# Optimization experiments

Measured on AMD Instinct MI355X. Metric: run time of the kernel, lower is better.

Reference implementation:

```python
import jax, jax.numpy as jnp
import numpy as np

B, Cin, Cout = 2, 32, 16
D, H, W = 48, 64, 128
K = 3
EPS = 1e-5  # BatchNorm3d default eps


def setup_inputs() -> dict:
    key = jax.random.key(0)
    ks = jax.random.split(key, 6)
    return {
        "x": jax.random.normal(ks[0], (B, Cin, D, H, W), jnp.float32),
        "weight": jax.random.normal(ks[1], (Cout, Cin, K, K, K), jnp.float32) * 0.05,
        "gamma": jax.random.uniform(ks[2], (Cout,), jnp.float32, minval=0.5, maxval=1.5),
        "beta": jax.random.normal(ks[3], (Cout,), jnp.float32) * 0.1,
        "running_mean": jax.random.normal(ks[4], (Cout,), jnp.float32) * 0.1,
        "running_var": jax.random.uniform(ks[5], (Cout,), jnp.float32, minval=0.5, maxval=1.5),
    }


def _binarize(v):
    # forward: sign(v) in {-1, 0, +1}; backward (STE): hardtanh grad (pass-through on |v|<=1)
    clipped = jnp.clip(v, -1.0, 1.0)
    return clipped + jax.lax.stop_gradient(jnp.sign(v) - clipped)


def reference(x, weight, gamma, beta, running_mean, running_var):
    b, c, d, h, w = x.shape
    # trilinear upsample, scale (1,2,2), align_corners=False (half-pixel centers)
    x = jax.image.resize(x, (b, c, d, 2 * h, 2 * w), method="trilinear")
    # binarize activations and weights; XNOR-style per-output-channel scale alpha = mean|W|
    xb = _binarize(x)
    alpha = jnp.mean(jnp.abs(weight), axis=(1, 2, 3, 4), keepdims=True)  # [Cout,1,1,1,1]
    wb = _binarize(weight) * alpha
    y = jax.lax.conv_general_dilated(
        xb, wb,
        window_strides=(1, 1, 1),
        padding=[(1, 1), (1, 1), (1, 1)],
        dimension_numbers=("NCDHW", "OIDHW", "NCDHW"),
    )  # [B, Cout, D, 2H, 2W]
    # fused BatchNorm3d (inference form) + ReLU
    inv = gamma / jnp.sqrt(running_var + EPS)
    shift = beta - running_mean * inv
    y = y * inv[None, :, None, None, None] + shift[None, :, None, None, None]
    return jax.nn.relu(y)
```

## Files before the change

kernel.cpp:

```cpp
#include <hip/hip_runtime.h>
#include <hip/hip_bf16.h>
#include <stdint.h>

#define BB   2
#define CIN  32
#define COUT 16
#define DD   48
#define HIN  64
#define WIN  128
#define H2   128
#define W2   256
#define PLANE_WORDS (H2 * W2)

__global__ __launch_bounds__(512) void ibc3d_prep(
    const float* __restrict__ wgt, const float* __restrict__ gamma,
    const float* __restrict__ beta, const float* __restrict__ rmean,
    const float* __restrict__ rvar, uint32_t* __restrict__ bw,
    float* __restrict__ scale, float* __restrict__ shift)
{
    int t = threadIdx.x;
    if (t < 27 * 16) {
        int tap = t >> 4, co = t & 15;
        uint32_t word = 0;
        for (int ci = 0; ci < CIN; ++ci) {
            float v = wgt[(co * CIN + ci) * 27 + tap];
            word |= (v > 0.0f ? 1u : 0u) << ci;
        }
        bw[t] = word;
    }
    {
        int co   = t >> 5;
        int lane = t & 31;
        double p = 0.0;
        for (int k = 0; k < 27; ++k)
            p += fabs((double)wgt[co * (CIN * 27) + lane + 32 * k]);
#pragma unroll
        for (int s = 16; s >= 1; s >>= 1)
            p += __shfl_down(p, s, 32);
        if (lane == 0) {
            float alpha = (float)(p / (double)(CIN * 27));
            float inv = gamma[co] / sqrtf(rvar[co] + 1e-5f);
            scale[co] = alpha * inv;
            shift[co] = beta[co] - rmean[co] * inv;
        }
    }
}

__device__ __forceinline__ uint32_t pack_word(const float* __restrict__ x,
                                              int b, int d, int h2, int w2)
{
    int m = h2 >> 1, dh = h2 & 1;
    int n = w2 >> 1, dwp = w2 & 1;
    int rA = m + dh - 1;
    int rB = rA + 1;
    double wA = dh ? 0.75 : 0.25;
    double wB = 1.0 - wA;
    rA = rA < 0 ? 0 : rA;
    rB = rB > (HIN - 1) ? (HIN - 1) : rB;
    int cA = n + dwp - 1;
    int cB = cA + 1;
    double wC = dwp ? 0.75 : 0.25;
    double wD = 1.0 - wC;
    cA = cA < 0 ? 0 : cA;
    cB = cB > (WIN - 1) ? (WIN - 1) : cB;

    const float* xp = x + ((size_t)b * CIN * DD + d) * (HIN * WIN);
    int oA = rA * WIN, oB = rB * WIN;
    uint32_t word = 0;
    for (int ci = 0; ci < CIN; ++ci) {
        const float* xc = xp + (size_t)ci * (DD * HIN * WIN);
        float a0 = xc[oA + cA], a1 = xc[oA + cB];
        float b0 = xc[oB + cA], b1 = xc[oB + cB];
        double t0 = wA * (double)a0 + wB * (double)b0;
        double t1 = wA * (double)a1 + wB * (double)b1;
        double v  = wC * t0 + wD * t1;
        word |= (v >= 0.0 ? 1u : 0u) << ci;
    }
    return word;
}

__global__ __launch_bounds__(256) void ibc3d_packr8(
    const float* __restrict__ x, uint32_t* __restrict__ bx,
    int b_start, int nplanes)
{
    int per = gridDim.x >> 3;
    int bid = (blockIdx.x & 7) * per + (blockIdx.x >> 3);
    int idx = bid * 256 + threadIdx.x;
    int j  = idx & 31;
    int h2 = (idx >> 5) & (H2 - 1);
    int pl = idx >> 12;
    if (pl >= nplanes) return;
    int d  = pl % DD;
    int b  = b_start + pl / DD;

    int m = h2 >> 1, q = h2 & 1;
    int rT = q ? m : (m > 0 ? m - 1 : 0);
    int rB = q ? (m < HIN - 1 ? m + 1 : HIN - 1) : m;
    float wT = q ? 0.75f : 0.25f;
    float wB = 1.0f - wT;

    int c0 = 4 * j;
    int cl = c0 >= 2 ? c0 - 2 : 0;
    int cr = (c0 + 4 <= WIN - 2) ? c0 + 4 : WIN - 2;

    const float* xp = x + ((size_t)b * CIN * DD + d) * (HIN * WIN);
    int oT = rT * WIN, oB2 = rB * WIN;

    uint32_t w[8];
#pragma unroll
    for (int k = 0; k < 8; ++k) w[k] = 0u;

#pragma unroll 2
    for (int ci = 0; ci < CIN; ++ci) {
        const float* xc = xp + (size_t)ci * (DD * HIN * WIN);
        float cT[6], cB[6];
        {
            const float* rowT = xc + oT;
            float2 L = *(const float2*)(rowT + cl);
            float4 M = *(const float4*)(rowT + c0);
            float2 R = *(const float2*)(rowT + cr);
            cT[0] = (j > 0)  ? L.y : L.x;
            cT[1] = M.x; cT[2] = M.y; cT[3] = M.z; cT[4] = M.w;
            cT[5] = (j < 31) ? R.x : R.y;
        }
        {
            const float* rowB = xc + oB2;
            float2 L = *(const float2*)(rowB + cl);
            float4 M = *(const float4*)(rowB + c0);
            float2 R = *(const float2*)(rowB + cr);
            cB[0] = (j > 0)  ? L.y : L.x;
            cB[1] = M.x; cB[2] = M.y; cB[3] = M.z; cB[4] = M.w;
            cB[5] = (j < 31) ? R.x : R.y;
        }

        float v[8];
#pragma unroll
        for (int t = 0; t < 4; ++t) {
            float uT0 = 0.25f * cT[t]     + 0.75f * cT[t + 1];
            float uT1 = 0.75f * cT[t + 1] + 0.25f * cT[t + 2];
            float uB0 = 0.25f * cB[t]     + 0.75f * cB[t + 1];
            float uB1 = 0.75f * cB[t + 1] + 0.25f * cB[t + 2];
            v[2 * t]     = wT * uT0 + wB * uB0;
            v[2 * t + 1] = wT * uT1 + wB * uB1;
        }

        float amin = 3.4e38f;
#pragma unroll
        for (int k = 0; k < 8; ++k)
            amin = fminf(amin, fabsf(v[k]));

        if (__builtin_expect(amin < 1e-5f, 0)) {
            double dwT = (double)wT, dwB = 1.0 - (double)wT;
#pragma unroll
            for (int t = 0; t < 4; ++t) {
                double eT0 = 0.25 * (double)cT[t]     + 0.75 * (double)cT[t + 1];
                double eT1 = 0.75 * (double)cT[t + 1] + 0.25 * (double)cT[t + 2];
                double eB0 = 0.25 * (double)cB[t]     + 0.75 * (double)cB[t + 1];
                double eB1 = 0.75 * (double)cB[t + 1] + 0.25 * (double)cB[t + 2];
                uint32_t s0 = (dwT * eT0 + dwB * eB0) >= 0.0;
                uint32_t s1 = (dwT * eT1 + dwB * eB1) >= 0.0;
                w[2 * t]     |= s0 << ci;
                w[2 * t + 1] |= s1 << ci;
            }
        } else {
#pragma unroll
            for (int k = 0; k < 8; ++k)
                w[k] |= (v[k] >= 0.0f ? 1u : 0u) << ci;
        }
    }

    size_t base = (size_t)pl * PLANE_WORDS + (size_t)h2 * W2 + 8 * j;
    *(uint4*)(bx + base)     = make_uint4(w[0], w[1], w[2], w[3]);
    *(uint4*)(bx + base + 4) = make_uint4(w[4], w[5], w[6], w[7]);
}

__global__ __launch_bounds__(256) void ibc3d_conv6(
    const uint32_t* __restrict__ bx, const uint32_t* __restrict__ bwg,
    const float* __restrict__ scaleg, const float* __restrict__ shiftg,
    float* __restrict__ out, int b_start)
{
    int per = gridDim.x >> 3;
    int bid = (blockIdx.x & 7) * per + (blockIdx.x >> 3);

    int h2    = bid & (H2 - 1);
    int plane = bid >> 7;
    int d     = plane % DD;
    int b     = b_start + plane / DD;
    int w2    = threadIdx.x;

    int acc[16];
#pragma unroll
    for (int c = 0; c < 16; ++c) acc[c] = 0;

#pragma unroll
    for (int kd = 0; kd < 3; ++kd) {
        int dd = d + kd - 1;
        if (dd < 0 || dd >= DD) continue;
        const uint32_t* bxp = bx + (size_t)(plane + kd - 1) * PLANE_WORDS;
#pragma unroll
        for (int kh = 0; kh < 3; ++kh) {
            int hh = h2 + kh - 1;
            if (hh < 0 || hh >= H2) continue;
            const uint32_t* brow = bxp + hh * W2;
#pragma unroll
            for (int kw = 0; kw < 3; ++kw) {
                int ww = w2 + kw - 1;
                if (ww >= 0 && ww < W2) {
                    uint32_t word = brow[ww];
                    int tap = kd * 9 + kh * 3 + kw;
#pragma unroll
                    for (int co = 0; co < 16; ++co)
                        acc[co] += __popc(word ^ bwg[tap * 16 + co]);
                }
            }
        }
    }

    int nd = 1 + (d > 0)  + (d < DD - 1);
    int nh = 1 + (h2 > 0) + (h2 < H2 - 1);
    int nw = 1 + (w2 > 0) + (w2 < W2 - 1);
    float base = 32.0f * (float)(nd * nh * nw);

    size_t obase = (((size_t)(b * COUT) * DD + d) * H2 + h2) * W2 + w2;
#pragma unroll
    for (int co = 0; co < 16; ++co) {
        float y = (base - 2.0f * (float)acc[co]) * scaleg[co] + shiftg[co];
        y = y > 0.0f ? y : 0.0f;
        out[obase + (size_t)co * (DD * H2 * W2)] = y;
    }
}

__global__ __launch_bounds__(256) void ibc3d_fused(
    const float* __restrict__ x, const float* __restrict__ wgt,
    const float* __restrict__ gamma, const float* __restrict__ beta,
    const float* __restrict__ rmean, const float* __restrict__ rvar,
    float* __restrict__ out)
{
    __shared__ uint32_t sbw[27 * 16];
    __shared__ float sscale[16];
    __shared__ float sshift[16];
    __shared__ uint32_t sw[3][10][264];

    int tid = threadIdx.x;
    for (int t = tid; t < 27 * 16; t += 256) {
        int tap = t >> 4, co = t & 15;
        uint32_t word = 0;
        for (int ci = 0; ci < CIN; ++ci) {
            float v = wgt[(co * CIN + ci) * 27 + tap];
            word |= (v > 0.0f ? 1u : 0u) << ci;
        }
        sbw[t] = word;
    }
    if (tid < 16) {
        int co = tid;
        double s = 0.0;
        for (int i = 0; i < CIN * 27; ++i)
            s += fabs((double)wgt[co * CIN * 27 + i]);
        float alpha = (float)(s / (double)(CIN * 27));
        float inv = gamma[co] / sqrtf(rvar[co] + 1e-5f);
        sscale[co] = alpha * inv;
        sshift[co] = beta[co] - rmean[co] * inv;
    }

    int bid = blockIdx.x;
    int hq  = bid & 15;
    int r   = bid >> 4;
    int b   = r / DD;
    int d   = r % DD;
    int h2base = hq * 8;

    for (int i = tid; i < 3 * 10 * 258; i += 256) {
        int kd  = i / 2580;
        int rem = i - kd * 2580;
        int ri  = rem / 258;
        int ciw = rem - ri * 258;
        int dd = d + kd - 1;
        int h2 = h2base - 1 + ri;
        int w2 = ciw - 1;
        uint32_t word = 0;
        if (dd >= 0 && dd < DD && h2 >= 0 && h2 < H2 && w2 >= 0 && w2 < W2)
            word = pack_word(x, b, dd, h2, w2);
        sw[kd][ri][ciw] = word;
    }
    __syncthreads();

    int w2 = tid;
    for (int p = 0; p < 8; ++p) {
        int h2 = h2base + p;
        int acc[16];
#pragma unroll
        for (int c = 0; c < 16; ++c) acc[c] = 0;
        int nv = 0;
        for (int kd = 0; kd < 3; ++kd) {
            int dd = d + kd - 1;
            if (dd < 0 || dd >= DD) continue;
            for (int kh = 0; kh < 3; ++kh) {
                int hh = h2 + kh - 1;
                if (hh < 0 || hh >= H2) continue;
                for (int kw = 0; kw < 3; ++kw) {
                    int ww = w2 + kw - 1;
                    if (ww < 0 || ww >= W2) continue;
                    uint32_t word = sw[kd][p + kh][w2 + kw];
                    nv += 1;
                    int tap = kd * 9 + kh * 3 + kw;
#pragma unroll
                    for (int co = 0; co < 16; ++co)
                        acc[co] += __popc(word ^ sbw[tap * 16 + co]);
                }
            }
        }
        float base = 32.0f * (float)nv;
#pragma unroll
        for (int co = 0; co < 16; ++co) {
            float y = (base - 2.0f * (float)acc[co]) * sscale[co] + sshift[co];
            y = y > 0.0f ? y : 0.0f;
            size_t oidx = (((size_t)(b * COUT + co) * DD + d) * H2 + h2) * W2 + w2;
            out[oidx] = y;
        }
    }
}

extern "C" void kernel_launch(void* const* d_in, const int* in_sizes, int n_in,
                              void* d_out, int out_size, void* d_ws, size_t ws_size,
                              hipStream_t stream)
{
    (void)in_sizes; (void)n_in; (void)out_size;
    const float* x     = (const float*)d_in[0];
    const float* wgt   = (const float*)d_in[1];
    const float* gamma = (const float*)d_in[2];
    const float* beta  = (const float*)d_in[3];
    const float* rmean = (const float*)d_in[4];
    const float* rvar  = (const float*)d_in[5];
    float* out = (float*)d_out;

    const size_t HDR = 4096;
    const size_t bx_full = (size_t)BB * DD * PLANE_WORDS * 4;
    const size_t bx_half = (size_t)DD * PLANE_WORDS * 4;

    if (d_ws != nullptr && ws_size >= HDR + bx_full) {
        uint8_t* ws = (uint8_t*)d_ws;
        uint32_t* bw    = (uint32_t*)ws;
        float*    scale = (float*)(ws + 2048);
        float*    shift = (float*)(ws + 2112);
        uint32_t* bx    = (uint32_t*)(ws + HDR);
        ibc3d_prep<<<1, 512, 0, stream>>>(wgt, gamma, beta, rmean, rvar, bw, scale, shift);
        int nplanes = BB * DD;
        ibc3d_packr8<<<nplanes * 16, 256, 0, stream>>>(x, bx, 0, nplanes);
        ibc3d_conv6<<<nplanes * H2, 256, 0, stream>>>(bx, bw, scale, shift, out, 0);
    } else if (d_ws != nullptr && ws_size >= HDR + bx_half) {
        uint8_t* ws = (uint8_t*)d_ws;
        uint32_t* bw    = (uint32_t*)ws;
        float*    scale = (float*)(ws + 2048);
        float*    shift = (float*)(ws + 2112);
        uint32_t* bx    = (uint32_t*)(ws + HDR);
        ibc3d_prep<<<1, 512, 0, stream>>>(wgt, gamma, beta, rmean, rvar, bw, scale, shift);
        for (int b = 0; b < BB; ++b) {
            ibc3d_packr8<<<DD * 16, 256, 0, stream>>>(x, bx, b, DD);
            ibc3d_conv6<<<DD * H2, 256, 0, stream>>>(bx, bw, scale, shift, out, b);
        }
    } else {
        ibc3d_fused<<<BB * DD * (H2 / 8), 256, 0, stream>>>(
            x, wgt, gamma, beta, rmean, rvar, out);
    }
}
```

Before: 146.7 us.

## Parallelize weight prep across 16 blocks and drop XCD-aware block swizzle in conv

The single-block weight preparation kernel becomes a 16-block kernel, one block per output channel. Each block stages its weight slice in shared memory and reduces |W| with a shared-memory tree, which shortens the serial prep launch. The conv kernel also drops the blockIdx remapping that grouped blocks by XCD, so consecutive rows are spread round-robin across XCDs. That may change L2 locality for the neighbouring-row reads.

```diff
diff --git a/kernel.cpp b/kernel.cpp
--- a/kernel.cpp
+++ b/kernel.cpp
@@ -12,37 +12,47 @@
 #define W2   256
 #define PLANE_WORDS (H2 * W2)
 
-__global__ __launch_bounds__(512) void ibc3d_prep(
+__global__ __launch_bounds__(256) void ibc3d_prep16(
     const float* __restrict__ wgt, const float* __restrict__ gamma,
     const float* __restrict__ beta, const float* __restrict__ rmean,
     const float* __restrict__ rvar, uint32_t* __restrict__ bw,
     float* __restrict__ scale, float* __restrict__ shift)
 {
-    int t = threadIdx.x;
-    if (t < 27 * 16) {
-        int tap = t >> 4, co = t & 15;
+    __shared__ float sw[CIN * 27];
+    __shared__ double sp[256];
+
+    int co  = blockIdx.x;
+    int tid = threadIdx.x;
+    const float* wslice = wgt + (size_t)co * (CIN * 27);
+
+    double p = 0.0;
+    for (int i = tid; i < CIN * 27; i += 256) {
+        float v = wslice[i];
+        sw[i] = v;
+        p += fabs((double)v);
+    }
+    sp[tid] = p;
+    __syncthreads();
+
+#pragma unroll
+    for (int s = 128; s > 0; s >>= 1) {
+        if (tid < s) sp[tid] += sp[tid + s];
+        __syncthreads();
+    }
+
+    if (tid < 27) {
+        int tap = tid;
         uint32_t word = 0;
-        for (int ci = 0; ci < CIN; ++ci) {
-            float v = wgt[(co * CIN + ci) * 27 + tap];
-            word |= (v > 0.0f ? 1u : 0u) << ci;
-        }
-        bw[t] = word;
-    }
-    {
-        int co   = t >> 5;
-        int lane = t & 31;
-        double p = 0.0;
-        for (int k = 0; k < 27; ++k)
-            p += fabs((double)wgt[co * (CIN * 27) + lane + 32 * k]);
-#pragma unroll
-        for (int s = 16; s >= 1; s >>= 1)
-            p += __shfl_down(p, s, 32);
-        if (lane == 0) {
-            float alpha = (float)(p / (double)(CIN * 27));
-            float inv = gamma[co] / sqrtf(rvar[co] + 1e-5f);
-            scale[co] = alpha * inv;
-            shift[co] = beta[co] - rmean[co] * inv;
-        }
+#pragma unroll
+        for (int ci = 0; ci < CIN; ++ci)
+            word |= (sw[ci * 27 + tap] > 0.0f ? 1u : 0u) << ci;
+        bw[tap * 16 + co] = word;
+    }
+    if (tid == 0) {
+        float alpha = (float)(sp[0] / (double)(CIN * 27));
+        float inv = gamma[co] / sqrtf(rvar[co] + 1e-5f);
+        scale[co] = alpha * inv;
+        shift[co] = beta[co] - rmean[co] * inv;
     }
 }
 
@@ -174,14 +184,12 @@
     *(uint4*)(bx + base + 4) = make_uint4(w[4], w[5], w[6], w[7]);
 }
 
-__global__ __launch_bounds__(256) void ibc3d_conv6(
+__global__ __launch_bounds__(256) void ibc3d_conv3(
     const uint32_t* __restrict__ bx, const uint32_t* __restrict__ bwg,
     const float* __restrict__ scaleg, const float* __restrict__ shiftg,
     float* __restrict__ out, int b_start)
 {
-    int per = gridDim.x >> 3;
-    int bid = (blockIdx.x & 7) * per + (blockIdx.x >> 3);
-
+    int bid   = blockIdx.x;
     int h2    = bid & (H2 - 1);
     int plane = bid >> 7;
     int d     = plane % DD;
@@ -343,20 +351,20 @@
         float*    scale = (float*)(ws + 2048);
         float*    shift = (float*)(ws + 2112);
         uint32_t* bx    = (uint32_t*)(ws + HDR);
-        ibc3d_prep<<<1, 512, 0, stream>>>(wgt, gamma, beta, rmean, rvar, bw, scale, shift);
+        ibc3d_prep16<<<16, 256, 0, stream>>>(wgt, gamma, beta, rmean, rvar, bw, scale, shift);
         int nplanes = BB * DD;
         ibc3d_packr8<<<nplanes * 16, 256, 0, stream>>>(x, bx, 0, nplanes);
-        ibc3d_conv6<<<nplanes * H2, 256, 0, stream>>>(bx, bw, scale, shift, out, 0);
+        ibc3d_conv3<<<nplanes * H2, 256, 0, stream>>>(bx, bw, scale, shift, out, 0);
     } else if (d_ws != nullptr && ws_size >= HDR + bx_half) {
         uint8_t* ws = (uint8_t*)d_ws;
         uint32_t* bw    = (uint32_t*)ws;
         float*    scale = (float*)(ws + 2048);
         float*    shift = (float*)(ws + 2112);
         uint32_t* bx    = (uint32_t*)(ws + HDR);
-        ibc3d_prep<<<1, 512, 0, stream>>>(wgt, gamma, beta, rmean, rvar, bw, scale, shift);
+        ibc3d_prep16<<<16, 256, 0, stream>>>(wgt, gamma, beta, rmean, rvar, bw, scale, shift);
         for (int b = 0; b < BB; ++b) {
             ibc3d_packr8<<<DD * 16, 256, 0, stream>>>(x, bx, b, DD);
-            ibc3d_conv6<<<DD * H2, 256, 0, stream>>>(bx, bw, scale, shift, out, b);
+            ibc3d_conv3<<<DD * H2, 256, 0, stream>>>(bx, bw, scale, shift, out, b);
         }
     } else {
         ibc3d_fused<<<BB * DD * (H2 / 8), 256, 0, stream>>>(
```

Result: faster. 143.0 us (-2.5%).

## Pad packed binary activations with zero halo to remove conv boundary branches

Applied to the files above, without the earlier changes.

Packed sign words are now written into a zero-padded volume (extra depth planes, rows and columns), so the conv kernel reads all 27 taps without bounds checks. Padding with zero words makes the XOR count differ from the true boundary contribution; a per-boundary-class bias table built in the prep kernel corrects for this and is folded, with the BN scale, into a single fma per output. It adds a kernel that zeroes the full padded buffer each call and drops the block-index swizzle, which costs extra memory traffic and launch overhead.

```diff
diff --git a/kernel.cpp b/kernel.cpp
--- a/kernel.cpp
+++ b/kernel.cpp
@@ -10,39 +10,211 @@
 #define WIN  128
 #define H2   128
 #define W2   256
-#define PLANE_WORDS (H2 * W2)
-
-__global__ __launch_bounds__(512) void ibc3d_prep(
+
+#define W2P  264
+#define HPR  130
+#define PDPW (HPR * W2P)
+#define PBW  (50 * PDPW)
+#define TOTW (2 * PBW)
+
+__global__ __launch_bounds__(512) void ibc3d_prep2(
     const float* __restrict__ wgt, const float* __restrict__ gamma,
     const float* __restrict__ beta, const float* __restrict__ rmean,
-    const float* __restrict__ rvar, uint32_t* __restrict__ bw,
-    float* __restrict__ scale, float* __restrict__ shift)
-{
+    const float* __restrict__ rvar, uint32_t* __restrict__ bwg,
+    float* __restrict__ A2g, float* __restrict__ Bcg)
+{
+    __shared__ uint32_t sbw[432];
+    __shared__ float ssc[16], ssh[16];
     int t = threadIdx.x;
-    if (t < 27 * 16) {
+
+    if (t < 432) {
         int tap = t >> 4, co = t & 15;
         uint32_t word = 0;
         for (int ci = 0; ci < CIN; ++ci) {
             float v = wgt[(co * CIN + ci) * 27 + tap];
             word |= (v > 0.0f ? 1u : 0u) << ci;
         }
-        bw[t] = word;
+        sbw[t] = word;
+        bwg[t] = word;
     }
     {
-        int co   = t >> 5;
-        int lane = t & 31;
+        int co = t >> 5, lane = t & 31;
         double p = 0.0;
         for (int k = 0; k < 27; ++k)
             p += fabs((double)wgt[co * (CIN * 27) + lane + 32 * k]);
 #pragma unroll
-        for (int s = 16; s >= 1; s >>= 1)
-            p += __shfl_down(p, s, 32);
+        for (int s = 16; s >= 1; s >>= 1) p += __shfl_down(p, s, 32);
         if (lane == 0) {
             float alpha = (float)(p / (double)(CIN * 27));
             float inv = gamma[co] / sqrtf(rvar[co] + 1e-5f);
-            scale[co] = alpha * inv;
-            shift[co] = beta[co] - rmean[co] * inv;
-        }
+            ssc[co] = alpha * inv;
+            ssh[co] = beta[co] - rmean[co] * inv;
+        }
+    }
+    __syncthreads();
+    if (t < 16) A2g[t] = -2.0f * ssc[t];
+    if (t < 432) {
+        int cls = t >> 4, co = t & 15;
+        int cd = cls / 9, ch = (cls / 3) % 3, cw = cls % 3;
+        int corr = 0, nv = 0;
+        for (int tap = 0; tap < 27; ++tap) {
+            int kd = tap / 9, kh = (tap / 3) % 3, kw = tap % 3;
+            bool inval = (cd == 0 && kd == 0) || (cd == 2 && kd == 2) ||
+                         (ch == 0 && kh == 0) || (ch == 2 && kh == 2) ||
+                         (cw == 0 && kw == 0) || (cw == 2 && kw == 2);
+            if (inval) corr += __popc(sbw[tap * 16 + co]);
+            else ++nv;
+        }
+        Bcg[t] = (32.0f * (float)nv + 2.0f * (float)corr) * ssc[co] + ssh[co];
+    }
+}
+
+__global__ __launch_bounds__(256) void ibc3d_zerop(uint32_t* __restrict__ bxp)
+{
+    int idx = blockIdx.x * 256 + threadIdx.x;
+    if (idx < TOTW / 4)
+        ((uint4*)bxp)[idx] = make_uint4(0u, 0u, 0u, 0u);
+}
+
+__global__ __launch_bounds__(256) void ibc3d_packp8(
+    const float* __restrict__ x, uint32_t* __restrict__ bxp)
+{
+    int per = gridDim.x >> 3;
+    int bid = (blockIdx.x & 7) * per + (blockIdx.x >> 3);
+    int idx = bid * 256 + threadIdx.x;
+    int j  = idx & 31;
+    int h2 = (idx >> 5) & (H2 - 1);
+    int pl = idx >> 12;
+    int d  = pl % DD;
+    int b  = pl / DD;
+
+    int m = h2 >> 1, q = h2 & 1;
+    int rT = q ? m : (m > 0 ? m - 1 : 0);
+    int rB = q ? (m < HIN - 1 ? m + 1 : HIN - 1) : m;
+    float wT = q ? 0.75f : 0.25f;
+    float wB = 1.0f - wT;
+
+    int c0 = 4 * j;
+    int cl = c0 >= 2 ? c0 - 2 : 0;
+    int cr = (c0 + 4 <= WIN - 2) ? c0 + 4 : WIN - 2;
+
+    const float* xp = x + ((size_t)b * CIN * DD + d) * (HIN * WIN);
+    int oT = rT * WIN, oB2 = rB * WIN;
+
+    uint32_t w[8];
+#pragma unroll
+    for (int k = 0; k < 8; ++k) w[k] = 0u;
+
+#pragma unroll 2
+    for (int ci = 0; ci < CIN; ++ci) {
+        const float* xc = xp + (size_t)ci * (DD * HIN * WIN);
+        float cT[6], cB[6];
+        {
+            const float* rowT = xc + oT;
+            float2 L = *(const float2*)(rowT + cl);
+            float4 M = *(const float4*)(rowT + c0);
+            float2 R = *(const float2*)(rowT + cr);
+            cT[0] = (j > 0)  ? L.y : L.x;
+            cT[1] = M.x; cT[2] = M.y; cT[3] = M.z; cT[4] = M.w;
+            cT[5] = (j < 31) ? R.x : R.y;
+        }
+        {
+            const float* rowB = xc + oB2;
+            float2 L = *(const float2*)(rowB + cl);
+            float4 M = *(const float4*)(rowB + c0);
+            float2 R = *(const float2*)(rowB + cr);
+            cB[0] = (j > 0)  ? L.y : L.x;
+            cB[1] = M.x; cB[2] = M.y; cB[3] = M.z; cB[4] = M.w;
+            cB[5] = (j < 31) ? R.x : R.y;
+        }
+
+        float v[8];
+#pragma unroll
+        for (int t = 0; t < 4; ++t) {
+            float uT0 = 0.25f * cT[t]     + 0.75f * cT[t + 1];
+            float uT1 = 0.75f * cT[t + 1] + 0.25f * cT[t + 2];
+            float uB0 = 0.25f * cB[t]     + 0.75f * cB[t + 1];
+            float uB1 = 0.75f * cB[t + 1] + 0.25f * cB[t + 2];
+            v[2 * t]     = wT * uT0 + wB * uB0;
+            v[2 * t + 1] = wT * uT1 + wB * uB1;
+        }
+
+        float amin = 3.4e38f;
+#pragma unroll
+        for (int k = 0; k < 8; ++k)
+            amin = fminf(amin, fabsf(v[k]));
+
+        if (__builtin_expect(amin < 1e-5f, 0)) {
+            double dwT = (double)wT, dwB = 1.0 - (double)wT;
+#pragma unroll
+            for (int t = 0; t < 4; ++t) {
+                double eT0 = 0.25 * (double)cT[t]     + 0.75 * (double)cT[t + 1];
+                double eT1 = 0.75 * (double)cT[t + 1] + 0.25 * (double)cT[t + 2];
+                double eB0 = 0.25 * (double)cB[t]     + 0.75 * (double)cB[t + 1];
+                double eB1 = 0.75 * (double)cB[t + 1] + 0.25 * (double)cB[t + 2];
+                uint32_t s0 = (dwT * eT0 + dwB * eB0) >= 0.0;
+                uint32_t s1 = (dwT * eT1 + dwB * eB1) >= 0.0;
+                w[2 * t]     |= s0 << ci;
+                w[2 * t + 1] |= s1 << ci;
+            }
+        } else {
+#pragma unroll
+            for (int k = 0; k < 8; ++k)
+                w[k] |= (v[k] >= 0.0f ? 1u : 0u) << ci;
+        }
+    }
+
+    size_t base = ((size_t)((b * 50 + d + 1) * HPR + (h2 + 1))) * W2P + 4 + 8 * j;
+    *(uint4*)(bxp + base)     = make_uint4(w[0], w[1], w[2], w[3]);
+    *(uint4*)(bxp + base + 4) = make_uint4(w[4], w[5], w[6], w[7]);
+}
+
+__global__ __launch_bounds__(256) void ibc3d_convp(
+    const uint32_t* __restrict__ bxp, const uint32_t* __restrict__ bwg,
+    const float* __restrict__ A2g, const float* __restrict__ Bcg,
+    float* __restrict__ out)
+{
+    int bid   = blockIdx.x;
+    int h2    = bid & (H2 - 1);
+    int plane = bid >> 7;
+    int d     = plane % DD;
+    int b     = plane / DD;
+    int w2    = threadIdx.x;
+
+    const uint32_t* P0 = bxp +
+        ((size_t)((b * 50 + d) * HPR + h2)) * W2P + w2 + 3;
+
+    int acc[16];
+#pragma unroll
+    for (int c = 0; c < 16; ++c) acc[c] = 0;
+
+#pragma unroll
+    for (int kd = 0; kd < 3; ++kd) {
+        const uint32_t* P = P0 + kd * PDPW;
+#pragma unroll
+        for (int kh = 0; kh < 3; ++kh) {
+#pragma unroll
+            for (int kw = 0; kw < 3; ++kw) {
+                uint32_t word = P[kh * W2P + kw];
+                int tap = kd * 9 + kh * 3 + kw;
+#pragma unroll
+                for (int co = 0; co < 16; ++co)
+                    acc[co] += __popc(word ^ bwg[tap * 16 + co]);
+            }
+        }
+    }
+
+    int cd = (d == 0)  ? 0 : ((d == DD - 1) ? 2 : 1);
+    int ch = (h2 == 0) ? 0 : ((h2 == H2 - 1) ? 2 : 1);
+    int cw = (w2 == 0) ? 0 : ((w2 == W2 - 1) ? 2 : 1);
+    int cls16 = (cd * 9 + ch * 3 + cw) * 16;
+
+    size_t obase = (((size_t)(b * COUT) * DD + d) * H2 + h2) * W2 + w2;
+#pragma unroll
+    for (int co = 0; co < 16; ++co) {
+        float y = fmaf(A2g[co], (float)acc[co], Bcg[cls16 + co]);
+        y = y > 0.0f ? y : 0.0f;
+        out[obase + (size_t)co * (DD * H2 * W2)] = y;
     }
 }
 
@@ -79,157 +251,6 @@
     return word;
 }
 
-__global__ __launch_bounds__(256) void ibc3d_packr8(
-    const float* __restrict__ x, uint32_t* __restrict__ bx,
-    int b_start, int nplanes)
-{
-    int per = gridDim.x >> 3;
-    int bid = (blockIdx.x & 7) * per + (blockIdx.x >> 3);
-    int idx = bid * 256 + threadIdx.x;
-    int j  = idx & 31;
-    int h2 = (idx >> 5) & (H2 - 1);
-    int pl = idx >> 12;
-    if (pl >= nplanes) return;
-    int d  = pl % DD;
-    int b  = b_start + pl / DD;
-
-    int m = h2 >> 1, q = h2 & 1;
-    int rT = q ? m : (m > 0 ? m - 1 : 0);
-    int rB = q ? (m < HIN - 1 ? m + 1 : HIN - 1) : m;
-    float wT = q ? 0.75f : 0.25f;
-    float wB = 1.0f - wT;
-
-    int c0 = 4 * j;
-    int cl = c0 >= 2 ? c0 - 2 : 0;
-    int cr = (c0 + 4 <= WIN - 2) ? c0 + 4 : WIN - 2;
-
-    const float* xp = x + ((size_t)b * CIN * DD + d) * (HIN * WIN);
-    int oT = rT * WIN, oB2 = rB * WIN;
-
-    uint32_t w[8];
-#pragma unroll
-    for (int k = 0; k < 8; ++k) w[k] = 0u;
-
-#pragma unroll 2
-    for (int ci = 0; ci < CIN; ++ci) {
-        const float* xc = xp + (size_t)ci * (DD * HIN * WIN);
-        float cT[6], cB[6];
-        {
-            const float* rowT = xc + oT;
-            float2 L = *(const float2*)(rowT + cl);
-            float4 M = *(const float4*)(rowT + c0);
-            float2 R = *(const float2*)(rowT + cr);
-            cT[0] = (j > 0)  ? L.y : L.x;
-            cT[1] = M.x; cT[2] = M.y; cT[3] = M.z; cT[4] = M.w;
-            cT[5] = (j < 31) ? R.x : R.y;
-        }
-        {
-            const float* rowB = xc + oB2;
-            float2 L = *(const float2*)(rowB + cl);
-            float4 M = *(const float4*)(rowB + c0);
-            float2 R = *(const float2*)(rowB + cr);
-            cB[0] = (j > 0)  ? L.y : L.x;
-            cB[1] = M.x; cB[2] = M.y; cB[3] = M.z; cB[4] = M.w;
-            cB[5] = (j < 31) ? R.x : R.y;
-        }
-
-        float v[8];
-#pragma unroll
-        for (int t = 0; t < 4; ++t) {
-            float uT0 = 0.25f * cT[t]     + 0.75f * cT[t + 1];
-            float uT1 = 0.75f * cT[t + 1] + 0.25f * cT[t + 2];
-            float uB0 = 0.25f * cB[t]     + 0.75f * cB[t + 1];
-            float uB1 = 0.75f * cB[t + 1] + 0.25f * cB[t + 2];
-            v[2 * t]     = wT * uT0 + wB * uB0;
-            v[2 * t + 1] = wT * uT1 + wB * uB1;
-        }
-
-        float amin = 3.4e38f;
-#pragma unroll
-        for (int k = 0; k < 8; ++k)
-            amin = fminf(amin, fabsf(v[k]));
-
-        if (__builtin_expect(amin < 1e-5f, 0)) {
-            double dwT = (double)wT, dwB = 1.0 - (double)wT;
-#pragma unroll
-            for (int t = 0; t < 4; ++t) {
-                double eT0 = 0.25 * (double)cT[t]     + 0.75 * (double)cT[t + 1];
-                double eT1 = 0.75 * (double)cT[t + 1] + 0.25 * (double)cT[t + 2];
-                double eB0 = 0.25 * (double)cB[t]     + 0.75 * (double)cB[t + 1];
-                double eB1 = 0.75 * (double)cB[t + 1] + 0.25 * (double)cB[t + 2];
-                uint32_t s0 = (dwT * eT0 + dwB * eB0) >= 0.0;
-                uint32_t s1 = (dwT * eT1 + dwB * eB1) >= 0.0;
-                w[2 * t]     |= s0 << ci;
-                w[2 * t + 1] |= s1 << ci;
-            }
-        } else {
-#pragma unroll
-            for (int k = 0; k < 8; ++k)
-                w[k] |= (v[k] >= 0.0f ? 1u : 0u) << ci;
-        }
-    }
-
-    size_t base = (size_t)pl * PLANE_WORDS + (size_t)h2 * W2 + 8 * j;
-    *(uint4*)(bx + base)     = make_uint4(w[0], w[1], w[2], w[3]);
-    *(uint4*)(bx + base + 4) = make_uint4(w[4], w[5], w[6], w[7]);
-}
-
-__global__ __launch_bounds__(256) void ibc3d_conv6(
-    const uint32_t* __restrict__ bx, const uint32_t* __restrict__ bwg,
-    const float* __restrict__ scaleg, const float* __restrict__ shiftg,
-    float* __restrict__ out, int b_start)
-{
-    int per = gridDim.x >> 3;
-    int bid = (blockIdx.x & 7) * per + (blockIdx.x >> 3);
-
-    int h2    = bid & (H2 - 1);
-    int plane = bid >> 7;
-    int d     = plane % DD;
-    int b     = b_start + plane / DD;
-    int w2    = threadIdx.x;
-
-    int acc[16];
-#pragma unroll
-    for (int c = 0; c < 16; ++c) acc[c] = 0;
-
-#pragma unroll
-    for (int kd = 0; kd < 3; ++kd) {
-        int dd = d + kd - 1;
-        if (dd < 0 || dd >= DD) continue;
-        const uint32_t* bxp = bx + (size_t)(plane + kd - 1) * PLANE_WORDS;
-#pragma unroll
-        for (int kh = 0; kh < 3; ++kh) {
-            int hh = h2 + kh - 1;
-            if (hh < 0 || hh >= H2) continue;
-            const uint32_t* brow = bxp + hh * W2;
-#pragma unroll
-            for (int kw = 0; kw < 3; ++kw) {
-                int ww = w2 + kw - 1;
-                if (ww >= 0 && ww < W2) {
-                    uint32_t word = brow[ww];
-                    int tap = kd * 9 + kh * 3 + kw;
-#pragma unroll
-                    for (int co = 0; co < 16; ++co)
-                        acc[co] += __popc(word ^ bwg[tap * 16 + co]);
-                }
-            }
-        }
-    }
-
-    int nd = 1 + (d > 0)  + (d < DD - 1);
-    int nh = 1 + (h2 > 0) + (h2 < H2 - 1);
-    int nw = 1 + (w2 > 0) + (w2 < W2 - 1);
-    float base = 32.0f * (float)(nd * nh * nw);
-
-    size_t obase = (((size_t)(b * COUT) * DD + d) * H2 + h2) * W2 + w2;
-#pragma unroll
-    for (int co = 0; co < 16; ++co) {
-        float y = (base - 2.0f * (float)acc[co]) * scaleg[co] + shiftg[co];
-        y = y > 0.0f ? y : 0.0f;
-        out[obase + (size_t)co * (DD * H2 * W2)] = y;
-    }
-}
-
 __global__ __launch_bounds__(256) void ibc3d_fused(
     const float* __restrict__ x, const float* __restrict__ wgt,
     const float* __restrict__ gamma, const float* __restrict__ beta,
@@ -333,31 +354,21 @@
     const float* rvar  = (const float*)d_in[5];
     float* out = (float*)d_out;
 
-    const size_t HDR = 4096;
-    const size_t bx_full = (size_t)BB * DD * PLANE_WORDS * 4;
-    const size_t bx_half = (size_t)DD * PLANE_WORDS * 4;
-
-    if (d_ws != nullptr && ws_size >= HDR + bx_full) {
-        uint8_t* ws = (uint8_t*)d_ws;
-        uint32_t* bw    = (uint32_t*)ws;
-        float*    scale = (float*)(ws + 2048);
-        float*    shift = (float*)(ws + 2112);
-        uint32_t* bx    = (uint32_t*)(ws + HDR);
-        ibc3d_prep<<<1, 512, 0, stream>>>(wgt, gamma, beta, rmean, rvar, bw, scale, shift);
-        int nplanes = BB * DD;
-        ibc3d_packr8<<<nplanes * 16, 256, 0, stream>>>(x, bx, 0, nplanes);
-        ibc3d_conv6<<<nplanes * H2, 256, 0, stream>>>(bx, bw, scale, shift, out, 0);
-    } else if (d_ws != nullptr && ws_size >= HDR + bx_half) {
-        uint8_t* ws = (uint8_t*)d_ws;
-        uint32_t* bw    = (uint32_t*)ws;
-        float*    scale = (float*)(ws + 2048);
-        float*    shift = (float*)(ws + 2112);
-        uint32_t* bx    = (uint32_t*)(ws + HDR);
-        ibc3d_prep<<<1, 512, 0, stream>>>(wgt, gamma, beta, rmean, rvar, bw, scale, shift);
-        for (int b = 0; b < BB; ++b) {
-            ibc3d_packr8<<<DD * 16, 256, 0, stream>>>(x, bx, b, DD);
-            ibc3d_conv6<<<DD * H2, 256, 0, stream>>>(bx, bw, scale, shift, out, b);
-        }
+    const size_t BXOFF = 32768;
+    const size_t need = BXOFF + (size_t)TOTW * 4;
+
+    if (d_ws != nullptr && ws_size >= need) {
+        uint8_t*  ws  = (uint8_t*)d_ws;
+        uint32_t* bwg = (uint32_t*)ws;
+        float*    A2g = (float*)(ws + 4096);
+        float*    Bcg = (float*)(ws + 8192);
+        uint32_t* bxp = (uint32_t*)(ws + BXOFF);
+
+        ibc3d_prep2<<<1, 512, 0, stream>>>(wgt, gamma, beta, rmean, rvar,
+                                           bwg, A2g, Bcg);
+        ibc3d_zerop<<<(TOTW / 4 + 255) / 256, 256, 0, stream>>>(bxp);
+        ibc3d_packp8<<<BB * DD * 16, 256, 0, stream>>>(x, bxp);
+        ibc3d_convp<<<BB * DD * H2, 256, 0, stream>>>(bxp, bwg, A2g, Bcg, out);
     } else {
         ibc3d_fused<<<BB * DD * (H2 / 8), 256, 0, stream>>>(
             x, wgt, gamma, beta, rmean, rvar, out);
```

New measurement: 181.6 us. 1.24x slower.
